# Optimization experiments

Measured on AMD Instinct MI355X. Metric: run time of the kernel, lower is better.

## Reference

```python
import jax, jax.numpy as jnp
import numpy as np

LAMDA_1 = 1.0
LAMDA_CLASS = 1.0
LAMDA_V = 1.0
B, F, C, T, N = 16384, 512, 2, 256, 256  # batch, slots, classes, target len, pred_v len


def setup_inputs() -> dict:
    key = jax.random.key(0)
    k1, k2, k3 = jax.random.split(key, 3)
    pred_class = jax.random.normal(k1, (B, 1, F, C), dtype=jnp.float32)
    # values near 1 so the length-N product (loss_multi term) stays numerically sane
    pred_v = 0.9 + 0.2 * jax.random.uniform(k2, (B, N), dtype=jnp.float32)
    targets = jax.random.uniform(k3, (B, T), dtype=jnp.float32)
    return {"pred_class": pred_class, "pred_v": pred_v, "targets": targets}


def reference(pred_class, pred_v, targets):
    logits = pred_class[:, 0]  # [B, F, C]

    # ---- loss_classify: CE against labels = 1 for first T slots, 0 after ----
    true_labels = (jnp.arange(F) < T).astype(jnp.int32)  # [F]
    logp = jax.nn.log_softmax(logits, axis=-1)  # [B, F, C]
    picked = jnp.take_along_axis(
        logp, jnp.broadcast_to(true_labels[None, :, None], (B, F, 1)), axis=2
    )[..., 0]  # [B, F]
    loss_label = (-picked.mean()) * LAMDA_CLASS

    # ---- loss_result ----
    pred_labels = jnp.argmax(logits, axis=-1)  # [B, F]
    multi_all = jnp.prod(pred_v, axis=1)  # [B]
    loss_multi = jnp.mean((multi_all - 1.0) ** 2) * LAMDA_1

    # match j-th positive class slot to t_count-th pred_v entry (running counter)
    mask = pred_labels[:, :T] == 1  # [B, T]
    idx = jnp.clip(jnp.cumsum(mask.astype(jnp.int32), axis=1) - 1, 0, N - 1)
    matched = jnp.take_along_axis(pred_v, idx, axis=1)  # [B, T]
    lossv1 = jnp.sum(jnp.where(mask, (matched - targets) ** 2, 0.0), axis=1)  # [B]
    t_count = jnp.sum(mask, axis=1).astype(jnp.float32)  # [B]
    has_match = t_count > 0
    # countt = f_count + t_count = T always (every j increments one counter)
    loss_true = jnp.mean(jnp.where(has_match, lossv1 / T, 0.0)) * LAMDA_V
    # pre == recall == t/T, so 2*p*r/(p+r) == t/T
    f1 = jnp.mean(jnp.where(has_match, t_count / T, 0.0))

    r = loss_multi + loss_true
    total_loss = loss_label + r
    return total_loss, loss_label, r, loss_multi, loss_true, f1
```

## Files before the change

kernel.cpp:

```cpp
#include <hip/hip_runtime.h>

#define B_TOT 16384
#define F_DIM 512
#define T_DIM 256
#define N_DIM 256
#define NBLK  2048

__device__ __forceinline__ float wave_sum(float v) {
#pragma unroll
    for (int o = 32; o; o >>= 1) v += __shfl_xor(v, o, 64);
    return v;
}
__device__ __forceinline__ float wave_prod(float v) {
#pragma unroll
    for (int o = 32; o; o >>= 1) v *= __shfl_xor(v, o, 64);
    return v;
}

__device__ __forceinline__ float lse2(float a, float b) {
    float m = fmaxf(a, b);
    return m + __logf(__expf(a - m) + __expf(b - m));
}

__global__ __launch_bounds__(256, 4) void setcrit_stage1(
    const float* __restrict__ pred_class,
    const float* __restrict__ pred_v,
    const float* __restrict__ targets,
    float* __restrict__ partial)
{
    __shared__ float s_predv[4][N_DIM];
    __shared__ float s_fin[4][4];

    const int tid = threadIdx.x;
    const int l   = tid & 63;
    const int w   = tid >> 6;
    const unsigned long long lt = (1ull << l) - 1ull;
    const int wave_id = blockIdx.x * 4 + w;

    float acc_pick = 0.f, acc_dsq = 0.f, acc_multi = 0.f;
    int   acc_tc = 0;

#pragma unroll
    for (int i = 0; i < 2; ++i) {
        const int b = i * (NBLK * 4) + wave_id;
        const float* lgp = pred_class + (size_t)b * (2 * F_DIM);
        const float* pvp = pred_v     + (size_t)b * N_DIM;
        const float* tgp = targets    + (size_t)b * T_DIM;

        float4 g0 = *(const float4*)(lgp + 8 * l);
        float4 g1 = *(const float4*)(lgp + 8 * l + 4);
        float4 g2 = *(const float4*)(lgp + 512 + 8 * l);
        float4 g3 = *(const float4*)(lgp + 512 + 8 * l + 4);
        float4 pv = *(const float4*)(pvp + 4 * l);
        float4 tg = *(const float4*)(tgp + 4 * l);

        *(float4*)(&s_predv[w][4 * l]) = pv;

        float p = 0.f;
        p += g0.y - lse2(g0.x, g0.y);
        p += g0.w - lse2(g0.z, g0.w);
        p += g1.y - lse2(g1.x, g1.y);
        p += g1.w - lse2(g1.z, g1.w);
        p += g2.x - lse2(g2.x, g2.y);
        p += g2.z - lse2(g2.z, g2.w);
        p += g3.x - lse2(g3.x, g3.y);
        p += g3.z - lse2(g3.z, g3.w);
        acc_pick += p;

        bool m0 = g0.y > g0.x;
        bool m1 = g0.w > g0.z;
        bool m2 = g1.y > g1.x;
        bool m3 = g1.w > g1.z;
        unsigned long long b0 = __ballot(m0);
        unsigned long long b1 = __ballot(m1);
        unsigned long long b2 = __ballot(m2);
        unsigned long long b3 = __ballot(m3);

        int e0 = __popcll(b0 & lt) + __popcll(b1 & lt)
               + __popcll(b2 & lt) + __popcll(b3 & lt);
        int e1 = e0 + (m0 ? 1 : 0);
        int e2 = e1 + (m1 ? 1 : 0);
        int e3 = e2 + (m2 ? 1 : 0);
        acc_tc += __popcll(b0) + __popcll(b1) + __popcll(b2) + __popcll(b3);

        float dsq = 0.f, d;
        if (m0) { d = s_predv[w][e0] - tg.x; dsq += d * d; }
        if (m1) { d = s_predv[w][e1] - tg.y; dsq += d * d; }
        if (m2) { d = s_predv[w][e2] - tg.z; dsq += d * d; }
        if (m3) { d = s_predv[w][e3] - tg.w; dsq += d * d; }
        acc_dsq += dsq;

        float prod = wave_prod(pv.x * pv.y * pv.z * pv.w);
        float pm1 = prod - 1.f;
        acc_multi += pm1 * pm1;
    }

    float pickS = wave_sum(acc_pick);
    float dsqS  = wave_sum(acc_dsq);
    if (l == 0) {
        s_fin[w][0] = pickS;
        s_fin[w][1] = acc_multi;
        s_fin[w][2] = dsqS;
        s_fin[w][3] = (float)acc_tc;
    }
    __syncthreads();
    if (tid == 0) {
        float v0 = 0.f, v1 = 0.f, v2 = 0.f, v3 = 0.f;
#pragma unroll
        for (int k = 0; k < 4; ++k) {
            v0 += s_fin[k][0]; v1 += s_fin[k][1];
            v2 += s_fin[k][2]; v3 += s_fin[k][3];
        }
        partial[0 * NBLK + blockIdx.x] = v0;
        partial[1 * NBLK + blockIdx.x] = v1;
        partial[2 * NBLK + blockIdx.x] = v2 * (1.f / (float)T_DIM);
        partial[3 * NBLK + blockIdx.x] = v3 * (1.f / (float)T_DIM);
    }
}

__global__ __launch_bounds__(256) void setcrit_stage2(
    const float* __restrict__ partial, float* __restrict__ out)
{
    __shared__ float s_red[4];
    const int tid = threadIdx.x;
    const int l   = tid & 63;
    const int w   = tid >> 6;

    float v = 0.f;
#pragma unroll
    for (int i = 0; i < NBLK / 64; ++i)
        v += partial[w * NBLK + i * 64 + l];
    v = wave_sum(v);
    if (l == 0) s_red[w] = v;
    __syncthreads();

    if (tid == 0) {
        float loss_label = -s_red[0] / ((float)B_TOT * (float)F_DIM);
        float loss_multi = s_red[1] / (float)B_TOT;
        float loss_true  = s_red[2] / (float)B_TOT;
        float f1         = s_red[3] / (float)B_TOT;
        float r = loss_multi + loss_true;
        out[0] = loss_label + r;
        out[1] = loss_label;
        out[2] = r;
        out[3] = loss_multi;
        out[4] = loss_true;
        out[5] = f1;
    }
}

extern "C" void kernel_launch(void* const* d_in, const int* in_sizes, int n_in,
                              void* d_out, int out_size, void* d_ws, size_t ws_size,
                              hipStream_t stream) {
    const float* pred_class = (const float*)d_in[0];
    const float* pred_v     = (const float*)d_in[1];
    const float* targets    = (const float*)d_in[2];
    float* partial = (float*)d_ws;

    setcrit_stage1<<<NBLK, 256, 0, stream>>>(pred_class, pred_v, targets, partial);
    setcrit_stage2<<<1, 256, 0, stream>>>(partial, (float*)d_out);
}
```

Measured before the change: 24.40 us.

## Hoist all row loads up front, simplify log-softmax pick, vectorize stage2 reduction

Stage 1 now issues every global load for both rows a wave handles before any compute, and pins them with empty asm so the compiler keeps them in flight together. It also gives each row its own shared pred_v buffer and drops the occupancy hint from launch bounds. The two-class log-softmax pick is rewritten as -log(1+exp(other-chosen)), which saves a max and an exp per pair but can lose precision or overflow for large logit gaps. Stage 2 reads the partials as float4 to cut load instructions; together these aim for more memory-level parallelism at the cost of higher register use.

```diff
diff --git a/kernel.cpp b/kernel.cpp
--- a/kernel.cpp
+++ b/kernel.cpp
@@ -6,6 +6,8 @@
 #define N_DIM 256
 #define NBLK  2048
 
+#define PIN4(v) asm volatile("" :: "v"((v).x), "v"((v).y), "v"((v).z), "v"((v).w))
+
 __device__ __forceinline__ float wave_sum(float v) {
 #pragma unroll
     for (int o = 32; o; o >>= 1) v += __shfl_xor(v, o, 64);
@@ -16,19 +18,17 @@
     for (int o = 32; o; o >>= 1) v *= __shfl_xor(v, o, 64);
     return v;
 }
-
-__device__ __forceinline__ float lse2(float a, float b) {
-    float m = fmaxf(a, b);
-    return m + __logf(__expf(a - m) + __expf(b - m));
-}
-
-__global__ __launch_bounds__(256, 4) void setcrit_stage1(
+__device__ __forceinline__ float pick_lp(float chosen, float other) {
+    return -__logf(1.f + __expf(other - chosen));
+}
+
+__global__ __launch_bounds__(256) void setcrit_stage1(
     const float* __restrict__ pred_class,
     const float* __restrict__ pred_v,
     const float* __restrict__ targets,
     float* __restrict__ partial)
 {
-    __shared__ float s_predv[4][N_DIM];
+    __shared__ float s_predv[2][4][N_DIM];
     __shared__ float s_fin[4][4];
 
     const int tid = threadIdx.x;
@@ -36,61 +36,110 @@
     const int w   = tid >> 6;
     const unsigned long long lt = (1ull << l) - 1ull;
     const int wave_id = blockIdx.x * 4 + w;
+    const int rA = wave_id;
+    const int rB = wave_id + NBLK * 4;
+
+    const float* lgA = pred_class + (size_t)rA * (2 * F_DIM);
+    const float* lgB = pred_class + (size_t)rB * (2 * F_DIM);
+
+    float4 a0 = *(const float4*)(lgA + 8 * l);
+    float4 a1 = *(const float4*)(lgA + 8 * l + 4);
+    float4 a2 = *(const float4*)(lgA + 512 + 8 * l);
+    float4 a3 = *(const float4*)(lgA + 512 + 8 * l + 4);
+    float4 pvA = *(const float4*)(pred_v  + (size_t)rA * N_DIM + 4 * l);
+    float4 tgA = *(const float4*)(targets + (size_t)rA * T_DIM + 4 * l);
+    float4 b0 = *(const float4*)(lgB + 8 * l);
+    float4 b1 = *(const float4*)(lgB + 8 * l + 4);
+    float4 b2 = *(const float4*)(lgB + 512 + 8 * l);
+    float4 b3 = *(const float4*)(lgB + 512 + 8 * l + 4);
+    float4 pvB = *(const float4*)(pred_v  + (size_t)rB * N_DIM + 4 * l);
+    float4 tgB = *(const float4*)(targets + (size_t)rB * T_DIM + 4 * l);
+
+    PIN4(a0); PIN4(a1); PIN4(a2); PIN4(a3); PIN4(pvA); PIN4(tgA);
+    PIN4(b0); PIN4(b1); PIN4(b2); PIN4(b3); PIN4(pvB); PIN4(tgB);
+
+    *(float4*)(&s_predv[0][w][4 * l]) = pvA;
+    *(float4*)(&s_predv[1][w][4 * l]) = pvB;
 
     float acc_pick = 0.f, acc_dsq = 0.f, acc_multi = 0.f;
     int   acc_tc = 0;
 
-#pragma unroll
-    for (int i = 0; i < 2; ++i) {
-        const int b = i * (NBLK * 4) + wave_id;
-        const float* lgp = pred_class + (size_t)b * (2 * F_DIM);
-        const float* pvp = pred_v     + (size_t)b * N_DIM;
-        const float* tgp = targets    + (size_t)b * T_DIM;
-
-        float4 g0 = *(const float4*)(lgp + 8 * l);
-        float4 g1 = *(const float4*)(lgp + 8 * l + 4);
-        float4 g2 = *(const float4*)(lgp + 512 + 8 * l);
-        float4 g3 = *(const float4*)(lgp + 512 + 8 * l + 4);
-        float4 pv = *(const float4*)(pvp + 4 * l);
-        float4 tg = *(const float4*)(tgp + 4 * l);
-
-        *(float4*)(&s_predv[w][4 * l]) = pv;
-
+    {
         float p = 0.f;
-        p += g0.y - lse2(g0.x, g0.y);
-        p += g0.w - lse2(g0.z, g0.w);
-        p += g1.y - lse2(g1.x, g1.y);
-        p += g1.w - lse2(g1.z, g1.w);
-        p += g2.x - lse2(g2.x, g2.y);
-        p += g2.z - lse2(g2.z, g2.w);
-        p += g3.x - lse2(g3.x, g3.y);
-        p += g3.z - lse2(g3.z, g3.w);
+        p += pick_lp(a0.y, a0.x);
+        p += pick_lp(a0.w, a0.z);
+        p += pick_lp(a1.y, a1.x);
+        p += pick_lp(a1.w, a1.z);
+        p += pick_lp(a2.x, a2.y);
+        p += pick_lp(a2.z, a2.w);
+        p += pick_lp(a3.x, a3.y);
+        p += pick_lp(a3.z, a3.w);
         acc_pick += p;
 
-        bool m0 = g0.y > g0.x;
-        bool m1 = g0.w > g0.z;
-        bool m2 = g1.y > g1.x;
-        bool m3 = g1.w > g1.z;
-        unsigned long long b0 = __ballot(m0);
-        unsigned long long b1 = __ballot(m1);
-        unsigned long long b2 = __ballot(m2);
-        unsigned long long b3 = __ballot(m3);
-
-        int e0 = __popcll(b0 & lt) + __popcll(b1 & lt)
-               + __popcll(b2 & lt) + __popcll(b3 & lt);
+        bool m0 = a0.y > a0.x;
+        bool m1 = a0.w > a0.z;
+        bool m2 = a1.y > a1.x;
+        bool m3 = a1.w > a1.z;
+        unsigned long long q0 = __ballot(m0);
+        unsigned long long q1 = __ballot(m1);
+        unsigned long long q2 = __ballot(m2);
+        unsigned long long q3 = __ballot(m3);
+
+        int e0 = __popcll(q0 & lt) + __popcll(q1 & lt)
+               + __popcll(q2 & lt) + __popcll(q3 & lt);
         int e1 = e0 + (m0 ? 1 : 0);
         int e2 = e1 + (m1 ? 1 : 0);
         int e3 = e2 + (m2 ? 1 : 0);
-        acc_tc += __popcll(b0) + __popcll(b1) + __popcll(b2) + __popcll(b3);
+        acc_tc += __popcll(q0) + __popcll(q1) + __popcll(q2) + __popcll(q3);
 
         float dsq = 0.f, d;
-        if (m0) { d = s_predv[w][e0] - tg.x; dsq += d * d; }
-        if (m1) { d = s_predv[w][e1] - tg.y; dsq += d * d; }
-        if (m2) { d = s_predv[w][e2] - tg.z; dsq += d * d; }
-        if (m3) { d = s_predv[w][e3] - tg.w; dsq += d * d; }
+        if (m0) { d = s_predv[0][w][e0] - tgA.x; dsq += d * d; }
+        if (m1) { d = s_predv[0][w][e1] - tgA.y; dsq += d * d; }
+        if (m2) { d = s_predv[0][w][e2] - tgA.z; dsq += d * d; }
+        if (m3) { d = s_predv[0][w][e3] - tgA.w; dsq += d * d; }
         acc_dsq += dsq;
 
-        float prod = wave_prod(pv.x * pv.y * pv.z * pv.w);
+        float prod = wave_prod(pvA.x * pvA.y * pvA.z * pvA.w);
+        float pm1 = prod - 1.f;
+        acc_multi += pm1 * pm1;
+    }
+
+    {
+        float p = 0.f;
+        p += pick_lp(b0.y, b0.x);
+        p += pick_lp(b0.w, b0.z);
+        p += pick_lp(b1.y, b1.x);
+        p += pick_lp(b1.w, b1.z);
+        p += pick_lp(b2.x, b2.y);
+        p += pick_lp(b2.z, b2.w);
+        p += pick_lp(b3.x, b3.y);
+        p += pick_lp(b3.z, b3.w);
+        acc_pick += p;
+
+        bool m0 = b0.y > b0.x;
+        bool m1 = b0.w > b0.z;
+        bool m2 = b1.y > b1.x;
+        bool m3 = b1.w > b1.z;
+        unsigned long long q0 = __ballot(m0);
+        unsigned long long q1 = __ballot(m1);
+        unsigned long long q2 = __ballot(m2);
+        unsigned long long q3 = __ballot(m3);
+
+        int e0 = __popcll(q0 & lt) + __popcll(q1 & lt)
+               + __popcll(q2 & lt) + __popcll(q3 & lt);
+        int e1 = e0 + (m0 ? 1 : 0);
+        int e2 = e1 + (m1 ? 1 : 0);
+        int e3 = e2 + (m2 ? 1 : 0);
+        acc_tc += __popcll(q0) + __popcll(q1) + __popcll(q2) + __popcll(q3);
+
+        float dsq = 0.f, d;
+        if (m0) { d = s_predv[1][w][e0] - tgB.x; dsq += d * d; }
+        if (m1) { d = s_predv[1][w][e1] - tgB.y; dsq += d * d; }
+        if (m2) { d = s_predv[1][w][e2] - tgB.z; dsq += d * d; }
+        if (m3) { d = s_predv[1][w][e3] - tgB.w; dsq += d * d; }
+        acc_dsq += dsq;
+
+        float prod = wave_prod(pvB.x * pvB.y * pvB.z * pvB.w);
         float pm1 = prod - 1.f;
         acc_multi += pm1 * pm1;
     }
@@ -126,11 +175,14 @@
     const int l   = tid & 63;
     const int w   = tid >> 6;
 
-    float v = 0.f;
-#pragma unroll
-    for (int i = 0; i < NBLK / 64; ++i)
-        v += partial[w * NBLK + i * 64 + l];
-    v = wave_sum(v);
+    const float4* p4 = (const float4*)(partial + w * NBLK);
+    float4 v4 = make_float4(0.f, 0.f, 0.f, 0.f);
+#pragma unroll
+    for (int i = 0; i < NBLK / 256; ++i) {
+        float4 t = p4[i * 64 + l];
+        v4.x += t.x; v4.y += t.y; v4.z += t.z; v4.w += t.w;
+    }
+    float v = wave_sum((v4.x + v4.y) + (v4.z + v4.w));
     if (l == 0) s_red[w] = v;
     __syncthreads();
 
```

Result: slower. 25.11 us (+2.9%).

## Batch four rows per wave with all loads hoisted, simplify log-softmax pick

Applied to the files above, without the earlier changes.

Halves the block count so each wave handles four batch rows and issues all of their global loads up front, raising memory-level parallelism. The per-row predv scratch gains a dimension, one per row. Two-class log-softmax is rewritten as -log(1+exp(other-chosen)), dropping a max and an exp. Stage 2 reads the smaller partial array with float4 loads. More registers per thread may lower occupancy, since the launch-bounds occupancy hint is removed.

```diff
diff --git a/kernel.cpp b/kernel.cpp
--- a/kernel.cpp
+++ b/kernel.cpp
@@ -4,7 +4,7 @@
 #define F_DIM 512
 #define T_DIM 256
 #define N_DIM 256
-#define NBLK  2048
+#define NBLK  1024
 
 __device__ __forceinline__ float wave_sum(float v) {
 #pragma unroll
@@ -16,19 +16,62 @@
     for (int o = 32; o; o >>= 1) v *= __shfl_xor(v, o, 64);
     return v;
 }
-
-__device__ __forceinline__ float lse2(float a, float b) {
-    float m = fmaxf(a, b);
-    return m + __logf(__expf(a - m) + __expf(b - m));
+__device__ __forceinline__ float pick_lp(float chosen, float other) {
+    return -__logf(1.f + __expf(other - chosen));
 }
 
-__global__ __launch_bounds__(256, 4) void setcrit_stage1(
+__device__ __forceinline__ void do_row(
+    const float4& g0, const float4& g1, const float4& g2, const float4& g3,
+    const float4& pv, const float4& tg, const float* __restrict__ pvlds,
+    unsigned long long lt,
+    float& acc_pick, float& acc_dsq, float& acc_multi, int& acc_tc)
+{
+    float p = 0.f;
+    p += pick_lp(g0.y, g0.x);
+    p += pick_lp(g0.w, g0.z);
+    p += pick_lp(g1.y, g1.x);
+    p += pick_lp(g1.w, g1.z);
+    p += pick_lp(g2.x, g2.y);
+    p += pick_lp(g2.z, g2.w);
+    p += pick_lp(g3.x, g3.y);
+    p += pick_lp(g3.z, g3.w);
+    acc_pick += p;
+
+    bool m0 = g0.y > g0.x;
+    bool m1 = g0.w > g0.z;
+    bool m2 = g1.y > g1.x;
+    bool m3 = g1.w > g1.z;
+    unsigned long long q0 = __ballot(m0);
+    unsigned long long q1 = __ballot(m1);
+    unsigned long long q2 = __ballot(m2);
+    unsigned long long q3 = __ballot(m3);
+
+    int e0 = __popcll(q0 & lt) + __popcll(q1 & lt)
+           + __popcll(q2 & lt) + __popcll(q3 & lt);
+    int e1 = e0 + (m0 ? 1 : 0);
+    int e2 = e1 + (m1 ? 1 : 0);
+    int e3 = e2 + (m2 ? 1 : 0);
+    acc_tc += __popcll(q0) + __popcll(q1) + __popcll(q2) + __popcll(q3);
+
+    float dsq = 0.f, d;
+    if (m0) { d = pvlds[e0] - tg.x; dsq += d * d; }
+    if (m1) { d = pvlds[e1] - tg.y; dsq += d * d; }
+    if (m2) { d = pvlds[e2] - tg.z; dsq += d * d; }
+    if (m3) { d = pvlds[e3] - tg.w; dsq += d * d; }
+    acc_dsq += dsq;
+
+    float prod = wave_prod(pv.x * pv.y * pv.z * pv.w);
+    float pm1 = prod - 1.f;
+    acc_multi += pm1 * pm1;
+}
+
+__global__ __launch_bounds__(256) void setcrit_stage1(
     const float* __restrict__ pred_class,
     const float* __restrict__ pred_v,
     const float* __restrict__ targets,
     float* __restrict__ partial)
 {
-    __shared__ float s_predv[4][N_DIM];
+    __shared__ float s_predv[4][4][N_DIM];
     __shared__ float s_fin[4][4];
 
     const int tid = threadIdx.x;
@@ -37,63 +80,31 @@
     const unsigned long long lt = (1ull << l) - 1ull;
     const int wave_id = blockIdx.x * 4 + w;
 
+    float4 g0[4], g1[4], g2[4], g3[4], pv[4], tg[4];
+
+#pragma unroll
+    for (int k = 0; k < 4; ++k) {
+        const int b = wave_id + k * (NBLK * 4);
+        const float* lgp = pred_class + (size_t)b * (2 * F_DIM);
+        g0[k] = *(const float4*)(lgp + 8 * l);
+        g1[k] = *(const float4*)(lgp + 8 * l + 4);
+        g2[k] = *(const float4*)(lgp + 512 + 8 * l);
+        g3[k] = *(const float4*)(lgp + 512 + 8 * l + 4);
+        pv[k] = *(const float4*)(pred_v  + (size_t)b * N_DIM + 4 * l);
+        tg[k] = *(const float4*)(targets + (size_t)b * T_DIM + 4 * l);
+    }
+
+#pragma unroll
+    for (int k = 0; k < 4; ++k)
+        *(float4*)(&s_predv[k][w][4 * l]) = pv[k];
+
     float acc_pick = 0.f, acc_dsq = 0.f, acc_multi = 0.f;
     int   acc_tc = 0;
 
 #pragma unroll
-    for (int i = 0; i < 2; ++i) {
-        const int b = i * (NBLK * 4) + wave_id;
-        const float* lgp = pred_class + (size_t)b * (2 * F_DIM);
-        const float* pvp = pred_v     + (size_t)b * N_DIM;
-        const float* tgp = targets    + (size_t)b * T_DIM;
-
-        float4 g0 = *(const float4*)(lgp + 8 * l);
-        float4 g1 = *(const float4*)(lgp + 8 * l + 4);
-        float4 g2 = *(const float4*)(lgp + 512 + 8 * l);
-        float4 g3 = *(const float4*)(lgp + 512 + 8 * l + 4);
-        float4 pv = *(const float4*)(pvp + 4 * l);
-        float4 tg = *(const float4*)(tgp + 4 * l);
-
-        *(float4*)(&s_predv[w][4 * l]) = pv;
-
-        float p = 0.f;
-        p += g0.y - lse2(g0.x, g0.y);
-        p += g0.w - lse2(g0.z, g0.w);
-        p += g1.y - lse2(g1.x, g1.y);
-        p += g1.w - lse2(g1.z, g1.w);
-        p += g2.x - lse2(g2.x, g2.y);
-        p += g2.z - lse2(g2.z, g2.w);
-        p += g3.x - lse2(g3.x, g3.y);
-        p += g3.z - lse2(g3.z, g3.w);
-        acc_pick += p;
-
-        bool m0 = g0.y > g0.x;
-        bool m1 = g0.w > g0.z;
-        bool m2 = g1.y > g1.x;
-        bool m3 = g1.w > g1.z;
-        unsigned long long b0 = __ballot(m0);
-        unsigned long long b1 = __ballot(m1);
-        unsigned long long b2 = __ballot(m2);
-        unsigned long long b3 = __ballot(m3);
-
-        int e0 = __popcll(b0 & lt) + __popcll(b1 & lt)
-               + __popcll(b2 & lt) + __popcll(b3 & lt);
-        int e1 = e0 + (m0 ? 1 : 0);
-        int e2 = e1 + (m1 ? 1 : 0);
-        int e3 = e2 + (m2 ? 1 : 0);
-        acc_tc += __popcll(b0) + __popcll(b1) + __popcll(b2) + __popcll(b3);
-
-        float dsq = 0.f, d;
-        if (m0) { d = s_predv[w][e0] - tg.x; dsq += d * d; }
-        if (m1) { d = s_predv[w][e1] - tg.y; dsq += d * d; }
-        if (m2) { d = s_predv[w][e2] - tg.z; dsq += d * d; }
-        if (m3) { d = s_predv[w][e3] - tg.w; dsq += d * d; }
-        acc_dsq += dsq;
-
-        float prod = wave_prod(pv.x * pv.y * pv.z * pv.w);
-        float pm1 = prod - 1.f;
-        acc_multi += pm1 * pm1;
-    }
+    for (int k = 0; k < 4; ++k)
+        do_row(g0[k], g1[k], g2[k], g3[k], pv[k], tg[k], s_predv[k][w],
+               lt, acc_pick, acc_dsq, acc_multi, acc_tc);
 
     float pickS = wave_sum(acc_pick);
     float dsqS  = wave_sum(acc_dsq);
@@ -126,11 +137,14 @@
     const int l   = tid & 63;
     const int w   = tid >> 6;
 
-    float v = 0.f;
+    const float4* p4 = (const float4*)(partial + w * NBLK);
+    float4 v4 = make_float4(0.f, 0.f, 0.f, 0.f);
 #pragma unroll
-    for (int i = 0; i < NBLK / 64; ++i)
-        v += partial[w * NBLK + i * 64 + l];
-    v = wave_sum(v);
+    for (int i = 0; i < NBLK / 256; ++i) {
+        float4 t = p4[i * 64 + l];
+        v4.x += t.x; v4.y += t.y; v4.z += t.z; v4.w += t.w;
+    }
+    float v = wave_sum((v4.x + v4.y) + (v4.z + v4.w));
     if (l == 0) s_red[w] = v;
     __syncthreads();
 
```

Result: slower. 25.56 us (+4.8%).
